# Kernel tuning notes

Measured on AMD Instinct MI355X. Metric: run time of the kernel, lower is better.

Reference implementation:

```python
import jax, jax.numpy as jnp
import numpy as np

ROPE_BASE = 100.0  # CroCo/InfiniteVGGT-style 2D RoPE base

def _rope_1d(sub, pos, base=ROPE_BASE):
    # sub: (B,H,N,half), pos: (B,N) float
    half = sub.shape[-1]
    quarter = half // 2
    inv_freq = 1.0 / (base ** (jnp.arange(quarter, dtype=jnp.float32) / quarter))
    ang = pos[:, None, :, None] * inv_freq  # (B,1,N,quarter)
    cos, sin = jnp.cos(ang), jnp.sin(ang)
    x1, x2 = sub[..., :quarter], sub[..., quarter:]
    return jnp.concatenate([x1 * cos - x2 * sin, x1 * sin + x2 * cos], axis=-1)

def rope_2d(t, positions):
    # t: (B,H,N,Dh); positions: (B,N,2) int (y,x)
    Dh = t.shape[-1]
    half = Dh // 2
    pos_f = positions.astype(t.dtype)
    y = _rope_1d(t[..., :half], pos_f[..., 0])
    x = _rope_1d(t[..., half:], pos_f[..., 1])
    return jnp.concatenate([y, x], axis=-1)

def setup_inputs() -> dict:
    key = jax.random.key(0)
    k1, k2, k3, k4 = jax.random.split(key, 4)
    B, N, C, H = 2, 2048, 1024, 16
    x = jax.random.normal(k1, (B, N, C), dtype=jnp.float32)
    positions = jax.random.randint(k2, (B, N, 2), 0, 64, dtype=jnp.int32)
    qkv_w = jax.random.normal(k3, (3 * C, C), dtype=jnp.float32) * (C ** -0.5)
    proj_w = jax.random.normal(k4, (C, C), dtype=jnp.float32) * (C ** -0.5)
    proj_b = jnp.zeros((C,), dtype=jnp.float32)
    return {"x": x, "positions": positions, "qkv_w": qkv_w, "proj_w": proj_w, "proj_b": proj_b}

def reference(x, positions, qkv_w, proj_w, proj_b):
    B, N, C = x.shape
    H = 16
    Dh = C // H
    scale = Dh ** -0.5
    qkv = (x @ qkv_w.T).reshape(B, N, 3, H, Dh).transpose(2, 0, 3, 1, 4)  # (3,B,H,N,Dh)
    q, k, v = qkv[0], qkv[1], qkv[2]
    q = rope_2d(q, positions)
    k = rope_2d(k, positions)
    attn = jnp.einsum('bhnd,bhmd->bhnm', q, k) * scale  # (B,H,N,N)
    attn = jax.nn.softmax(attn, axis=-1)
    out = jnp.einsum('bhnm,bhmd->bhnd', attn, v)  # (B,H,N,Dh)
    out = out.transpose(0, 2, 1, 3).reshape(B, N, C)
    return out @ proj_w.T + proj_b
```

## Files before the change

### kernel.cpp

```cpp
#include <hip/hip_runtime.h>
#include <cmath>

typedef unsigned short u16;
typedef unsigned int   u32;
typedef __attribute__((ext_vector_type(8))) __bf16 bf16x8;
typedef __attribute__((ext_vector_type(2))) __bf16 bf16x2;
typedef __attribute__((ext_vector_type(4))) float  f32x4;
typedef __attribute__((ext_vector_type(2))) unsigned int u32x2;

constexpr int BB = 2, SEQ = 2048, CH = 1024, NH = 16, DH = 64;

__device__ inline u16 f2bf(float f) {
    u32 u = __builtin_bit_cast(u32, f);
    u += 0x7FFF + ((u >> 16) & 1);
    return (u16)(u >> 16);
}
__device__ inline float bf2f(u16 b) { return __builtin_bit_cast(float, (u32)b << 16); }
__device__ inline u32 pkbf(float a, float b) {
#if __has_builtin(__builtin_amdgcn_cvt_pk_bf16_f32)
    bf16x2 r = __builtin_amdgcn_cvt_pk_bf16_f32(a, b);
    return __builtin_bit_cast(u32, r);
#else
    return (u32)f2bf(a) | ((u32)f2bf(b) << 16);
#endif
}
__device__ inline float fexp2(float x) {
#if __has_builtin(__builtin_amdgcn_exp2f)
    return __builtin_amdgcn_exp2f(x);
#else
    return exp2f(x);
#endif
}

__device__ inline void pl32swap(u32& a, u32& b) {
#if __has_builtin(__builtin_amdgcn_permlane32_swap)
    u32x2 r = __builtin_amdgcn_permlane32_swap(a, b, false, false);
    a = r.x; b = r.y;
#else
    const int ln = threadIdx.x & 63;
    u32 ax = (u32)__shfl_xor((int)a, 32), bx = (u32)__shfl_xor((int)b, 32);
    u32 na = (ln & 32) ? bx : a;
    u32 nb = (ln & 32) ? b : ax;
    a = na; b = nb;
#endif
}
__device__ inline void pl16swap(u32& a, u32& b) {
#if __has_builtin(__builtin_amdgcn_permlane16_swap)
    u32x2 r = __builtin_amdgcn_permlane16_swap(a, b, false, false);
    a = r.x; b = r.y;
#else
    const int ln = threadIdx.x & 63;
    u32 ax = (u32)__shfl_xor((int)a, 16), bx = (u32)__shfl_xor((int)b, 16);
    u32 na = (ln & 16) ? bx : a;
    u32 nb = (ln & 16) ? b : ax;
    a = na; b = nb;
#endif
}

__device__ inline void gld_lds16(const void* g, void* l) {
    __builtin_amdgcn_global_load_lds((const __attribute__((address_space(1))) void*)g,
                                     (__attribute__((address_space(3))) void*)l, 16, 0, 0);
}
__device__ inline f32x4 mfma16(bf16x8 a, bf16x8 b, f32x4 c) {
    return __builtin_amdgcn_mfma_f32_16x16x32_bf16(a, b, c, 0, 0, 0);
}
__device__ inline bf16x8 ld_frag(const u16* p) {
    return __builtin_bit_cast(bf16x8, *(const uint4*)p);
}

__global__ __launch_bounds__(256) void convert_kernel(const float* __restrict__ x,
                                                      const float* __restrict__ wq,
                                                      const float* __restrict__ wp,
                                                      u16* __restrict__ xb,
                                                      u16* __restrict__ wqb,
                                                      u16* __restrict__ wpb,
                                                      float2* __restrict__ tabq,
                                                      float2* __restrict__ tabk) {
    const int q = blockIdx.x * 256 + threadIdx.x;
    if (q >= 2097152) {
        const int idx = q - 2097152;
        if (idx < 1024) {
            const int p = idx >> 4, i = idx & 15;
            const float f = exp2f(-(float)i * 0.41524101186092f);
            float s, c;
            sincosf((float)p * f, &s, &c);
            tabk[idx] = make_float2(c, s);
            tabq[idx] = make_float2(c * 0.18033688011112042f,
                                    s * 0.18033688011112042f);
        }
        return;
    }
    const float* src; u16* dst; int idx;
    if (q < 1048576)            { src = x;  dst = xb;  idx = q; }
    else if (q < 1048576+786432){ src = wq; dst = wqb; idx = q - 1048576; }
    else                        { src = wp; dst = wpb; idx = q - 1048576 - 786432; }
    float4 v = *(const float4*)(src + (size_t)idx * 4);
    ushort4 o; o.x = f2bf(v.x); o.y = f2bf(v.y); o.z = f2bf(v.z); o.w = f2bf(v.w);
    *(ushort4*)(dst + (size_t)idx * 4) = o;
}

__global__ __launch_bounds__(256) void gemm_qkv_rope(const u16* __restrict__ A,
                                                     const u16* __restrict__ Bw,
                                                     const int* __restrict__ pos,
                                                     const float2* __restrict__ tabq,
                                                     const float2* __restrict__ tabk,
                                                     u16* __restrict__ Qb,
                                                     u16* __restrict__ Kb,
                                                     u16* __restrict__ Vt) {
    __shared__ u16 smem[18432];
    const int t = threadIdx.x, lane = t & 63, w = t >> 6;
    const int l15 = lane & 15, quad = lane >> 4;
    const int wm = w >> 1, wn = w & 1;
    const int m0 = blockIdx.y * 128, n0 = blockIdx.x * 128;
    const int K = CH;

    const int row0 = t >> 2, v0 = t & 3;
    const int gi0 = (v0 - (row0 >> 1)) & 3;
    const int row1 = row0 + 64;
    const int gi1 = (v0 - (row1 >> 1)) & 3;

    const u16* A0 = A  + (size_t)(m0 + row0) * K + gi0 * 8;
    const u16* A1 = A  + (size_t)(m0 + row1) * K + gi1 * 8;
    const u16* B0 = Bw + (size_t)(n0 + row0) * K + gi0 * 8;
    const u16* B1 = Bw + (size_t)(n0 + row1) * K + gi1 * 8;

    gld_lds16(A0, smem + t * 8);
    gld_lds16(A1, smem + 2048 + t * 8);
    gld_lds16(B0, smem + 8192 + t * 8);
    gld_lds16(B1, smem + 10240 + t * 8);

    f32x4 acc[4][4] = {};
    for (int kt = 0; kt < K / 32; ++kt) {
        __syncthreads();
        const int cur = (kt & 1) * 4096;
        if (kt + 1 < K / 32) {
            const int off = (kt + 1) * 32;
            const int nxt = ((kt + 1) & 1) * 4096;
            gld_lds16(A0 + off, smem + nxt + t * 8);
            gld_lds16(A1 + off, smem + nxt + 2048 + t * 8);
            gld_lds16(B0 + off, smem + 8192 + nxt + t * 8);
            gld_lds16(B1 + off, smem + 8192 + nxt + 2048 + t * 8);
        }
        const u16* as = smem + cur;
        const u16* bs = smem + 8192 + cur;
        bf16x8 af[4], bfv[4];
#pragma unroll
        for (int mi = 0; mi < 4; ++mi) {
            const int r = wm * 64 + mi * 16 + l15;
            af[mi] = ld_frag(as + (r * 4 + ((quad + (r >> 1)) & 3)) * 8);
        }
#pragma unroll
        for (int nj = 0; nj < 4; ++nj) {
            const int r = wn * 64 + nj * 16 + l15;
            bfv[nj] = ld_frag(bs + (r * 4 + ((quad + (r >> 1)) & 3)) * 8);
        }
#pragma unroll
        for (int mi = 0; mi < 4; ++mi)
#pragma unroll
            for (int nj = 0; nj < 4; ++nj)
                acc[mi][nj] = mfma16(af[mi], bfv[nj], acc[mi][nj]);
    }

    const int reg = n0 >> 10;
    const int h   = ((n0 & 1023) >> 6) + wn;
    __syncthreads();
    u16* T = smem + w * 4608;
    const int rsel = lane >> 3, csel = lane & 7;
    if (reg < 2) {
        const float2* tab = reg ? tabk : tabq;
        u16* dstb = reg ? Kb : Qb;
#pragma unroll
        for (int mi = 0; mi < 4; ++mi) {
#pragma unroll
            for (int r = 0; r < 4; ++r) {
                const int m = m0 + wm * 64 + mi * 16 + quad * 4 + r;
                const int2 pp = *(const int2*)(pos + m * 2);
                const float2 ty = tab[pp.x * 16 + l15];
                const float2 tx = tab[pp.y * 16 + l15];
                const float x1 = acc[mi][0][r], x2 = acc[mi][1][r];
                const float y1 = acc[mi][2][r], y2 = acc[mi][3][r];
                const int ml = (mi * 16 + quad * 4 + r) * 72;
                T[ml + l15]      = f2bf(x1 * ty.x - x2 * ty.y);
                T[ml + l15 + 16] = f2bf(x1 * ty.y + x2 * ty.x);
                T[ml + l15 + 32] = f2bf(y1 * tx.x - y2 * tx.y);
                T[ml + l15 + 48] = f2bf(y1 * tx.y + y2 * tx.x);
            }
        }
        const int mbase = m0 + wm * 64;
        const int bh = (mbase >> 11) * NH + h;
        const int nbase = mbase & 2047;
#pragma unroll
        for (int j = 0; j < 8; ++j) {
            const int row = rsel + j * 8;
            u16* gp = dstb + ((size_t)bh * SEQ + nbase + row) * 64 + csel * 8;
            *(uint4*)gp = *(const uint4*)&T[row * 72 + csel * 8];
        }
    } else {
#pragma unroll
        for (int mi = 0; mi < 4; ++mi)
#pragma unroll
            for (int nj = 0; nj < 4; ++nj)
#pragma unroll
                for (int r = 0; r < 4; ++r)
                    T[(nj * 16 + l15) * 72 + mi * 16 + quad * 4 + r] =
                        f2bf(acc[mi][nj][r]);
        const int bh = (m0 >> 11) * NH + h;
        const int nbase = (m0 & 2047) + wm * 64;
#pragma unroll
        for (int j = 0; j < 8; ++j) {
            const int d = rsel + j * 8;
            u16* gp = Vt + ((size_t)bh * 64 + d) * SEQ + nbase + csel * 8;
            *(uint4*)gp = *(const uint4*)&T[d * 72 + csel * 8];
        }
    }
}

__global__ __launch_bounds__(256, 4) void attn_mfma(const u16* __restrict__ Qb,
                                                    const u16* __restrict__ Kb,
                                                    const u16* __restrict__ Vt,
                                                    u16* __restrict__ Opart,
                                                    float* __restrict__ lpart) {
    __shared__ u16 Ks[2][4096];
    __shared__ u16 Vs[2][4096];
    const int t = threadIdx.x, lane = t & 63, w = t >> 6;
    const int l15 = lane & 15, quad = lane >> 4;
    const int bh = blockIdx.y;
    const int q0 = blockIdx.x * 128;
    const int z  = blockIdx.z;

    const int rowA = t >> 3, vA = t & 7;
    const int giA = (vA - rowA) & 7;
    const int rowB = rowA + 32;
    const int giB = (vA - rowB) & 7;

    const size_t kbase = (size_t)bh * SEQ * 64;
    const size_t vbase = (size_t)bh * 64 * SEQ;

    const uint4 ones_u = {0x3F803F80u, 0x3F803F80u, 0x3F803F80u, 0x3F803F80u};
    const bf16x8 onesf = __builtin_bit_cast(bf16x8, ones_u);

    bf16x8 aq[2][2];
#pragma unroll
    for (int mi = 0; mi < 2; ++mi)
#pragma unroll
        for (int ks = 0; ks < 2; ++ks)
            aq[mi][ks] = ld_frag(Qb + ((size_t)bh * SEQ + q0 + w * 32 + mi * 16 + l15) * 64
                                 + ks * 32 + quad * 8);

#define STAGE(kt_, buf_)                                                          \
    {                                                                             \
        const int k0_ = z * 1024 + (kt_) * 64;                                    \
        gld_lds16(Kb + kbase + (size_t)(k0_ + rowA) * 64 + giA * 8,               \
                  &Ks[buf_][t * 8]);                                              \
        gld_lds16(Kb + kbase + (size_t)(k0_ + rowB) * 64 + giB * 8,               \
                  &Ks[buf_][2048 + t * 8]);                                       \
        gld_lds16(Vt + vbase + (size_t)rowA * SEQ + k0_ + giA * 8,                \
                  &Vs[buf_][t * 8]);                                              \
        gld_lds16(Vt + vbase + (size_t)rowB * SEQ + k0_ + giB * 8,                \
                  &Vs[buf_][2048 + t * 8]);                                       \
    }

    STAGE(0, 0)

    f32x4 oacc[2][4] = {};
    f32x4 lacc[2] = {};

    for (int kt = 0; kt < 16; ++kt) {
        __syncthreads();
        if (kt + 1 < 16) STAGE(kt + 1, (kt + 1) & 1)
        const u16* ksm = Ks[kt & 1];
        const u16* vsm = Vs[kt & 1];

        f32x4 sacc[2][4] = {};
        __builtin_amdgcn_s_setprio(1);
#pragma unroll
        for (int ks = 0; ks < 2; ++ks)
#pragma unroll
            for (int nk = 0; nk < 4; ++nk) {
                const int rK = nk * 16 + l15;
                const bf16x8 kf = ld_frag(ksm + (rK * 8 + (((ks * 4 + quad) + rK) & 7)) * 8);
                sacc[0][nk] = mfma16(kf, aq[0][ks], sacc[0][nk]);
                sacc[1][nk] = mfma16(kf, aq[1][ks], sacc[1][nk]);
            }
        __builtin_amdgcn_s_setprio(0);

        bf16x8 pa[2][2];
#pragma unroll
        for (int mi = 0; mi < 2; ++mi) {
            u32 W[4][2];
#pragma unroll
            for (int nk = 0; nk < 4; ++nk) {
                const float p0 = fexp2(sacc[mi][nk][0]);
                const float p1 = fexp2(sacc[mi][nk][1]);
                const float p2 = fexp2(sacc[mi][nk][2]);
                const float p3 = fexp2(sacc[mi][nk][3]);
                W[nk][0] = pkbf(p0, p1);
                W[nk][1] = pkbf(p2, p3);
            }
            u32 t0[4], t1[4];
            {
                u32 a = W[0][0], c = W[1][0];
                pl32swap(a, c); pl16swap(a, c);
                t0[0] = a; t0[2] = c;
            }
            {
                u32 a = W[0][1], c = W[1][1];
                pl32swap(a, c); pl16swap(a, c);
                t0[1] = a; t0[3] = c;
            }
            {
                u32 a = W[2][0], c = W[3][0];
                pl32swap(a, c); pl16swap(a, c);
                t1[0] = a; t1[2] = c;
            }
            {
                u32 a = W[2][1], c = W[3][1];
                pl32swap(a, c); pl16swap(a, c);
                t1[1] = a; t1[3] = c;
            }
            uint4 u0; u0.x = t0[0]; u0.y = t0[1]; u0.z = t0[2]; u0.w = t0[3];
            uint4 u1; u1.x = t1[0]; u1.y = t1[1]; u1.z = t1[2]; u1.w = t1[3];
            pa[mi][0] = __builtin_bit_cast(bf16x8, u0);
            pa[mi][1] = __builtin_bit_cast(bf16x8, u1);
        }

        __builtin_amdgcn_s_setprio(1);
        lacc[0] = mfma16(pa[0][0], onesf, lacc[0]);
        lacc[0] = mfma16(pa[0][1], onesf, lacc[0]);
        lacc[1] = mfma16(pa[1][0], onesf, lacc[1]);
        lacc[1] = mfma16(pa[1][1], onesf, lacc[1]);
#pragma unroll
        for (int ks = 0; ks < 2; ++ks)
#pragma unroll
            for (int nj = 0; nj < 4; ++nj) {
                const int rV = nj * 16 + l15;
                const bf16x8 vf = ld_frag(vsm + (rV * 8 + (((ks * 4 + quad) + rV) & 7)) * 8);
                oacc[0][nj] = mfma16(pa[0][ks], vf, oacc[0][nj]);
                oacc[1][nj] = mfma16(pa[1][ks], vf, oacc[1][nj]);
            }
        __builtin_amdgcn_s_setprio(0);
    }
#undef STAGE

#pragma unroll
    for (int mi = 0; mi < 2; ++mi)
#pragma unroll
        for (int r = 0; r < 4; ++r) {
            const int qrow = q0 + w * 32 + mi * 16 + quad * 4 + r;
            if (l15 == 0)
                lpart[((size_t)z * 32 + bh) * SEQ + qrow] = lacc[mi][r];
            const size_t orow = (((size_t)z * 32 + bh) * SEQ + qrow) * 64;
#pragma unroll
            for (int nj = 0; nj < 4; ++nj)
                Opart[orow + nj * 16 + l15] = f2bf(oacc[mi][nj][r]);
        }
}

__global__ __launch_bounds__(256) void merge_kernel(const u16* __restrict__ Opart,
                                                    const float* __restrict__ lpart,
                                                    u16* __restrict__ Ob) {
    const int gid = blockIdx.x * 256 + threadIdx.x;
    const int d4 = gid & 15, q = (gid >> 4) & 2047, bh = gid >> 15;
    const size_t i1 = ((size_t)bh * SEQ + q) * 64 + d4 * 4;
    const size_t i2 = i1 + (size_t)32 * SEQ * 64;
    const float inv = 1.0f / (lpart[(size_t)bh * SEQ + q] +
                              lpart[(size_t)(32 + bh) * SEQ + q]);
    const ushort4 a = *(const ushort4*)(Opart + i1);
    const ushort4 b = *(const ushort4*)(Opart + i2);
    ushort4 o;
    o.x = f2bf((bf2f(a.x) + bf2f(b.x)) * inv);
    o.y = f2bf((bf2f(a.y) + bf2f(b.y)) * inv);
    o.z = f2bf((bf2f(a.z) + bf2f(b.z)) * inv);
    o.w = f2bf((bf2f(a.w) + bf2f(b.w)) * inv);
    const int b_ = bh >> 4, h = bh & 15;
    *(ushort4*)(Ob + ((size_t)(b_ * SEQ + q)) * CH + h * 64 + d4 * 4) = o;
}

__global__ __launch_bounds__(256) void gemm_proj(const u16* __restrict__ A,
                                                 const u16* __restrict__ Bw,
                                                 const float* __restrict__ bias,
                                                 float* __restrict__ C) {
    __shared__ u16 smem[12288];
    const int t = threadIdx.x, lane = t & 63, w = t >> 6;
    const int l15 = lane & 15, quad = lane >> 4;
    const int wm = w >> 1, wn = w & 1;
    const int m0 = blockIdx.y * 64, n0 = blockIdx.x * 128;
    const int K = CH, N = CH;

    const int row0 = t >> 2, v0 = t & 3;
    const int gi0 = (v0 - (row0 >> 1)) & 3;
    const int row1 = row0 + 64;
    const int gi1 = (v0 - (row1 >> 1)) & 3;

    const u16* A0 = A  + (size_t)(m0 + row0) * K + gi0 * 8;
    const u16* B0 = Bw + (size_t)(n0 + row0) * K + gi0 * 8;
    const u16* B1 = Bw + (size_t)(n0 + row1) * K + gi1 * 8;

    gld_lds16(A0, smem + t * 8);
    gld_lds16(B0, smem + 4096 + t * 8);
    gld_lds16(B1, smem + 4096 + 2048 + t * 8);

    f32x4 acc[2][4] = {};
    for (int kt = 0; kt < K / 32; ++kt) {
        __syncthreads();
        const int curA = (kt & 1) * 2048;
        const int curB = 4096 + (kt & 1) * 4096;
        if (kt + 1 < K / 32) {
            const int off = (kt + 1) * 32;
            const int nxtA = ((kt + 1) & 1) * 2048;
            const int nxtB = 4096 + ((kt + 1) & 1) * 4096;
            gld_lds16(A0 + off, smem + nxtA + t * 8);
            gld_lds16(B0 + off, smem + nxtB + t * 8);
            gld_lds16(B1 + off, smem + nxtB + 2048 + t * 8);
        }
        const u16* as = smem + curA;
        const u16* bs = smem + curB;
        bf16x8 af[2], bfv[4];
#pragma unroll
        for (int mi = 0; mi < 2; ++mi) {
            const int r = wm * 32 + mi * 16 + l15;
            af[mi] = ld_frag(as + (r * 4 + ((quad + (r >> 1)) & 3)) * 8);
        }
#pragma unroll
        for (int nj = 0; nj < 4; ++nj) {
            const int r = wn * 64 + nj * 16 + l15;
            bfv[nj] = ld_frag(bs + (r * 4 + ((quad + (r >> 1)) & 3)) * 8);
        }
#pragma unroll
        for (int mi = 0; mi < 2; ++mi)
#pragma unroll
            for (int nj = 0; nj < 4; ++nj)
                acc[mi][nj] = mfma16(af[mi], bfv[nj], acc[mi][nj]);
    }
#pragma unroll
    for (int mi = 0; mi < 2; ++mi)
#pragma unroll
        for (int nj = 0; nj < 4; ++nj) {
            const int n = n0 + wn * 64 + nj * 16 + l15;
            const float bv = bias[n];
#pragma unroll
            for (int r = 0; r < 4; ++r) {
                const int m = m0 + wm * 32 + mi * 16 + quad * 4 + r;
                C[(size_t)m * N + n] = acc[mi][nj][r] + bv;
            }
        }
}

extern "C" void kernel_launch(void* const* d_in, const int* in_sizes, int n_in,
                              void* d_out, int out_size, void* d_ws, size_t ws_size,
                              hipStream_t stream) {
    const float* x      = (const float*)d_in[0];
    const int*   pos    = (const int*)d_in[1];
    const float* qkv_w  = (const float*)d_in[2];
    const float* proj_w = (const float*)d_in[3];
    const float* proj_b = (const float*)d_in[4];
    float* out = (float*)d_out;

    u16* ws = (u16*)d_ws;
    u16* x_bf    = ws;
    u16* attn_bf = ws;
    u16* wq_bf   = ws + 4194304;
    float* lpart = (float*)(ws + 4194304);
    u16* wp_bf   = ws + 7340032;
    u16* Qb      = ws + 8388608;
    u16* Kb      = ws + 12582912;
    u16* Vt      = ws + 16777216;
    u16* Opart   = ws + 20971520;
    float2* tabq = (float2*)(ws + 20971520);
    float2* tabk = (float2*)(ws + 20971520 + 4096);

    const int M = BB * SEQ;

    convert_kernel<<<8196, 256, 0, stream>>>(x, qkv_w, proj_w, x_bf, wq_bf, wp_bf,
                                             tabq, tabk);
    gemm_qkv_rope<<<dim3(3 * CH / 128, M / 128), 256, 0, stream>>>(
        x_bf, wq_bf, pos, tabq, tabk, Qb, Kb, Vt);
    attn_mfma<<<dim3(SEQ / 128, BB * NH, 2), 256, 0, stream>>>(Qb, Kb, Vt, Opart, lpart);
    merge_kernel<<<4096, 256, 0, stream>>>(Opart, lpart, attn_bf);
    gemm_proj<<<dim3(CH / 128, M / 64), 256, 0, stream>>>(
        attn_bf, wp_bf, proj_b, out);
}
```

Measured before the change: 196.6 us.

## Split attention KV range four ways with XCD-aware block remap and 4-way merge

Splits the attention key/value sequence into four 512-length chunks instead of two, launching 2048 blocks with a flattened index remapped so consecutive blocks spread across groups (likely to match XCD placement and L2 reuse). Partial outputs go to two buffers, one reusing the output tensor as scratch, and the merge kernel now sums four partials and four row sums. It also raises the occupancy hint to 5 blocks per CU. This trades more partial-output traffic and merge work for more parallelism and shorter per-block loops.

```diff
diff --git a/kernel.cpp b/kernel.cpp
--- a/kernel.cpp
+++ b/kernel.cpp
@@ -215,18 +215,24 @@
     }
 }
 
-__global__ __launch_bounds__(256, 4) void attn_mfma(const u16* __restrict__ Qb,
+__global__ __launch_bounds__(256, 5) void attn_mfma(const u16* __restrict__ Qb,
                                                     const u16* __restrict__ Kb,
                                                     const u16* __restrict__ Vt,
-                                                    u16* __restrict__ Opart,
+                                                    u16* __restrict__ Op01,
+                                                    u16* __restrict__ Op23,
                                                     float* __restrict__ lpart) {
     __shared__ u16 Ks[2][4096];
     __shared__ u16 Vs[2][4096];
     const int t = threadIdx.x, lane = t & 63, w = t >> 6;
     const int l15 = lane & 15, quad = lane >> 4;
-    const int bh = blockIdx.y;
-    const int q0 = blockIdx.x * 128;
-    const int z  = blockIdx.z;
+
+    const int id = blockIdx.x;
+    const int c  = id & 7, r = id >> 3;
+    const int j  = r >> 4, xq = r & 15;
+    const int g  = c + 8 * j;
+    const int bh = g & 31;
+    const int z  = g >> 5;
+    const int q0 = xq * 128;
 
     const int rowA = t >> 3, vA = t & 7;
     const int giA = (vA - rowA) & 7;
@@ -249,7 +255,7 @@
 
 #define STAGE(kt_, buf_)                                                          \
     {                                                                             \
-        const int k0_ = z * 1024 + (kt_) * 64;                                    \
+        const int k0_ = z * 512 + (kt_) * 64;                                     \
         gld_lds16(Kb + kbase + (size_t)(k0_ + rowA) * 64 + giA * 8,               \
                   &Ks[buf_][t * 8]);                                              \
         gld_lds16(Kb + kbase + (size_t)(k0_ + rowB) * 64 + giB * 8,               \
@@ -265,9 +271,9 @@
     f32x4 oacc[2][4] = {};
     f32x4 lacc[2] = {};
 
-    for (int kt = 0; kt < 16; ++kt) {
+    for (int kt = 0; kt < 8; ++kt) {
         __syncthreads();
-        if (kt + 1 < 16) STAGE(kt + 1, (kt + 1) & 1)
+        if (kt + 1 < 8) STAGE(kt + 1, (kt + 1) & 1)
         const u16* ksm = Ks[kt & 1];
         const u16* vsm = Vs[kt & 1];
 
@@ -299,24 +305,24 @@
             }
             u32 t0[4], t1[4];
             {
-                u32 a = W[0][0], c = W[1][0];
-                pl32swap(a, c); pl16swap(a, c);
-                t0[0] = a; t0[2] = c;
+                u32 a = W[0][0], cc = W[1][0];
+                pl32swap(a, cc); pl16swap(a, cc);
+                t0[0] = a; t0[2] = cc;
             }
             {
-                u32 a = W[0][1], c = W[1][1];
-                pl32swap(a, c); pl16swap(a, c);
-                t0[1] = a; t0[3] = c;
+                u32 a = W[0][1], cc = W[1][1];
+                pl32swap(a, cc); pl16swap(a, cc);
+                t0[1] = a; t0[3] = cc;
             }
             {
-                u32 a = W[2][0], c = W[3][0];
-                pl32swap(a, c); pl16swap(a, c);
-                t1[0] = a; t1[2] = c;
+                u32 a = W[2][0], cc = W[3][0];
+                pl32swap(a, cc); pl16swap(a, cc);
+                t1[0] = a; t1[2] = cc;
             }
             {
-                u32 a = W[2][1], c = W[3][1];
-                pl32swap(a, c); pl16swap(a, c);
-                t1[1] = a; t1[3] = c;
+                u32 a = W[2][1], cc = W[3][1];
+                pl32swap(a, cc); pl16swap(a, cc);
+                t1[1] = a; t1[3] = cc;
             }
             uint4 u0; u0.x = t0[0]; u0.y = t0[1]; u0.z = t0[2]; u0.w = t0[3];
             uint4 u1; u1.x = t1[0]; u1.y = t1[1]; u1.z = t1[2]; u1.w = t1[3];
@@ -342,6 +348,7 @@
     }
 #undef STAGE
 
+    u16* ob = (z < 2 ? Op01 : Op23) + (size_t)(z & 1) * 4194304;
 #pragma unroll
     for (int mi = 0; mi < 2; ++mi)
 #pragma unroll
@@ -349,29 +356,33 @@
             const int qrow = q0 + w * 32 + mi * 16 + quad * 4 + r;
             if (l15 == 0)
                 lpart[((size_t)z * 32 + bh) * SEQ + qrow] = lacc[mi][r];
-            const size_t orow = (((size_t)z * 32 + bh) * SEQ + qrow) * 64;
+            const size_t orow = ((size_t)bh * SEQ + qrow) * 64;
 #pragma unroll
             for (int nj = 0; nj < 4; ++nj)
-                Opart[orow + nj * 16 + l15] = f2bf(oacc[mi][nj][r]);
-        }
-}
-
-__global__ __launch_bounds__(256) void merge_kernel(const u16* __restrict__ Opart,
+                ob[orow + nj * 16 + l15] = f2bf(oacc[mi][nj][r]);
+        }
+}
+
+__global__ __launch_bounds__(256) void merge_kernel(const u16* __restrict__ Op01,
+                                                    const u16* __restrict__ Op23,
                                                     const float* __restrict__ lpart,
                                                     u16* __restrict__ Ob) {
     const int gid = blockIdx.x * 256 + threadIdx.x;
     const int d4 = gid & 15, q = (gid >> 4) & 2047, bh = gid >> 15;
-    const size_t i1 = ((size_t)bh * SEQ + q) * 64 + d4 * 4;
-    const size_t i2 = i1 + (size_t)32 * SEQ * 64;
+    const size_t ibase = ((size_t)bh * SEQ + q) * 64 + d4 * 4;
     const float inv = 1.0f / (lpart[(size_t)bh * SEQ + q] +
-                              lpart[(size_t)(32 + bh) * SEQ + q]);
-    const ushort4 a = *(const ushort4*)(Opart + i1);
-    const ushort4 b = *(const ushort4*)(Opart + i2);
+                              lpart[((size_t)32 + bh) * SEQ + q] +
+                              lpart[((size_t)64 + bh) * SEQ + q] +
+                              lpart[((size_t)96 + bh) * SEQ + q]);
+    const ushort4 a = *(const ushort4*)(Op01 + ibase);
+    const ushort4 b = *(const ushort4*)(Op01 + ibase + 4194304);
+    const ushort4 cc = *(const ushort4*)(Op23 + ibase);
+    const ushort4 d = *(const ushort4*)(Op23 + ibase + 4194304);
     ushort4 o;
-    o.x = f2bf((bf2f(a.x) + bf2f(b.x)) * inv);
-    o.y = f2bf((bf2f(a.y) + bf2f(b.y)) * inv);
-    o.z = f2bf((bf2f(a.z) + bf2f(b.z)) * inv);
-    o.w = f2bf((bf2f(a.w) + bf2f(b.w)) * inv);
+    o.x = f2bf((bf2f(a.x) + bf2f(b.x) + bf2f(cc.x) + bf2f(d.x)) * inv);
+    o.y = f2bf((bf2f(a.y) + bf2f(b.y) + bf2f(cc.y) + bf2f(d.y)) * inv);
+    o.z = f2bf((bf2f(a.z) + bf2f(b.z) + bf2f(cc.z) + bf2f(d.z)) * inv);
+    o.w = f2bf((bf2f(a.w) + bf2f(b.w) + bf2f(cc.w) + bf2f(d.w)) * inv);
     const int b_ = bh >> 4, h = bh & 15;
     *(ushort4*)(Ob + ((size_t)(b_ * SEQ + q)) * CH + h * 64 + d4 * 4) = o;
 }
@@ -458,14 +469,15 @@
 
     u16* ws = (u16*)d_ws;
     u16* x_bf    = ws;
-    u16* attn_bf = ws;
     u16* wq_bf   = ws + 4194304;
     float* lpart = (float*)(ws + 4194304);
     u16* wp_bf   = ws + 7340032;
     u16* Qb      = ws + 8388608;
+    u16* attn_bf = ws + 8388608;
     u16* Kb      = ws + 12582912;
     u16* Vt      = ws + 16777216;
-    u16* Opart   = ws + 20971520;
+    u16* Op01    = ws + 20971520;
+    u16* Op23    = (u16*)d_out;
     float2* tabq = (float2*)(ws + 20971520);
     float2* tabk = (float2*)(ws + 20971520 + 4096);
 
@@ -475,8 +487,8 @@
                                              tabq, tabk);
     gemm_qkv_rope<<<dim3(3 * CH / 128, M / 128), 256, 0, stream>>>(
         x_bf, wq_bf, pos, tabq, tabk, Qb, Kb, Vt);
-    attn_mfma<<<dim3(SEQ / 128, BB * NH, 2), 256, 0, stream>>>(Qb, Kb, Vt, Opart, lpart);
-    merge_kernel<<<4096, 256, 0, stream>>>(Opart, lpart, attn_bf);
+    attn_mfma<<<2048, 256, 0, stream>>>(Qb, Kb, Vt, Op01, Op23, lpart);
+    merge_kernel<<<4096, 256, 0, stream>>>(Op01, Op23, lpart, attn_bf);
     gemm_proj<<<dim3(CH / 128, M / 64), 256, 0, stream>>>(
         attn_bf, wp_bf, proj_b, out);
 }
```

After: 265.1 us. +34.9%, slower.

## Shrink attention query tile, drop double buffering, remap 1D grid for XCD locality

Applied to the files above, without the earlier changes.

The attention kernel now processes 64 query rows per block instead of 128, with each wave handling 16 rows. It loads K/V tiles into a single LDS buffer with two barriers per iteration instead of double-buffering. The grid becomes a 1D launch of 2048 blocks, with a swizzled index so blocks sharing the same head and split land on the same XCD, and occupancy is raised to 8 blocks per CU. The intent is more waves in flight and better L2 reuse of K/V, at the cost of twice the K/V traffic per query and an exposed load latency with no prefetch.

```diff
diff --git a/kernel.cpp b/kernel.cpp
--- a/kernel.cpp
+++ b/kernel.cpp
@@ -215,18 +215,23 @@
     }
 }
 
-__global__ __launch_bounds__(256, 4) void attn_mfma(const u16* __restrict__ Qb,
+__global__ __launch_bounds__(256, 8) void attn_mfma(const u16* __restrict__ Qb,
                                                     const u16* __restrict__ Kb,
                                                     const u16* __restrict__ Vt,
                                                     u16* __restrict__ Opart,
                                                     float* __restrict__ lpart) {
-    __shared__ u16 Ks[2][4096];
-    __shared__ u16 Vs[2][4096];
+    __shared__ u16 Ks[4096];
+    __shared__ u16 Vs[4096];
     const int t = threadIdx.x, lane = t & 63, w = t >> 6;
     const int l15 = lane & 15, quad = lane >> 4;
-    const int bh = blockIdx.y;
-    const int q0 = blockIdx.x * 128;
-    const int z  = blockIdx.z;
+
+    const int id = blockIdx.x;
+    const int c  = id & 7, r_ = id >> 3;
+    const int j  = r_ >> 5, xq = r_ & 31;
+    const int g  = c + 8 * j;
+    const int bh = g & 31;
+    const int z  = g >> 5;
+    const int q0 = xq * 64;
 
     const int rowA = t >> 3, vA = t & 7;
     const int giA = (vA - rowA) & 7;
@@ -239,121 +244,110 @@
     const uint4 ones_u = {0x3F803F80u, 0x3F803F80u, 0x3F803F80u, 0x3F803F80u};
     const bf16x8 onesf = __builtin_bit_cast(bf16x8, ones_u);
 
-    bf16x8 aq[2][2];
-#pragma unroll
-    for (int mi = 0; mi < 2; ++mi)
-#pragma unroll
-        for (int ks = 0; ks < 2; ++ks)
-            aq[mi][ks] = ld_frag(Qb + ((size_t)bh * SEQ + q0 + w * 32 + mi * 16 + l15) * 64
-                                 + ks * 32 + quad * 8);
-
-#define STAGE(kt_, buf_)                                                          \
+    bf16x8 aq[2];
+#pragma unroll
+    for (int ks = 0; ks < 2; ++ks)
+        aq[ks] = ld_frag(Qb + ((size_t)bh * SEQ + q0 + w * 16 + l15) * 64
+                         + ks * 32 + quad * 8);
+
+#define STAGE(kt_)                                                                \
     {                                                                             \
         const int k0_ = z * 1024 + (kt_) * 64;                                    \
         gld_lds16(Kb + kbase + (size_t)(k0_ + rowA) * 64 + giA * 8,               \
-                  &Ks[buf_][t * 8]);                                              \
+                  &Ks[t * 8]);                                                    \
         gld_lds16(Kb + kbase + (size_t)(k0_ + rowB) * 64 + giB * 8,               \
-                  &Ks[buf_][2048 + t * 8]);                                       \
+                  &Ks[2048 + t * 8]);                                             \
         gld_lds16(Vt + vbase + (size_t)rowA * SEQ + k0_ + giA * 8,                \
-                  &Vs[buf_][t * 8]);                                              \
+                  &Vs[t * 8]);                                                    \
         gld_lds16(Vt + vbase + (size_t)rowB * SEQ + k0_ + giB * 8,                \
-                  &Vs[buf_][2048 + t * 8]);                                       \
-    }
-
-    STAGE(0, 0)
-
-    f32x4 oacc[2][4] = {};
-    f32x4 lacc[2] = {};
+                  &Vs[2048 + t * 8]);                                             \
+    }
+
+    f32x4 oacc[4] = {};
+    f32x4 lacc = {};
 
     for (int kt = 0; kt < 16; ++kt) {
         __syncthreads();
-        if (kt + 1 < 16) STAGE(kt + 1, (kt + 1) & 1)
-        const u16* ksm = Ks[kt & 1];
-        const u16* vsm = Vs[kt & 1];
-
-        f32x4 sacc[2][4] = {};
+        STAGE(kt)
+        __syncthreads();
+
+        f32x4 sacc[4] = {};
         __builtin_amdgcn_s_setprio(1);
 #pragma unroll
         for (int ks = 0; ks < 2; ++ks)
 #pragma unroll
             for (int nk = 0; nk < 4; ++nk) {
                 const int rK = nk * 16 + l15;
-                const bf16x8 kf = ld_frag(ksm + (rK * 8 + (((ks * 4 + quad) + rK) & 7)) * 8);
-                sacc[0][nk] = mfma16(kf, aq[0][ks], sacc[0][nk]);
-                sacc[1][nk] = mfma16(kf, aq[1][ks], sacc[1][nk]);
+                const bf16x8 kf = ld_frag(Ks + (rK * 8 + (((ks * 4 + quad) + rK) & 7)) * 8);
+                sacc[nk] = mfma16(kf, aq[ks], sacc[nk]);
             }
         __builtin_amdgcn_s_setprio(0);
 
-        bf16x8 pa[2][2];
-#pragma unroll
-        for (int mi = 0; mi < 2; ++mi) {
+        bf16x8 pa[2];
+        {
             u32 W[4][2];
 #pragma unroll
             for (int nk = 0; nk < 4; ++nk) {
-                const float p0 = fexp2(sacc[mi][nk][0]);
-                const float p1 = fexp2(sacc[mi][nk][1]);
-                const float p2 = fexp2(sacc[mi][nk][2]);
-                const float p3 = fexp2(sacc[mi][nk][3]);
+                const float p0 = fexp2(sacc[nk][0]);
+                const float p1 = fexp2(sacc[nk][1]);
+                const float p2 = fexp2(sacc[nk][2]);
+                const float p3 = fexp2(sacc[nk][3]);
                 W[nk][0] = pkbf(p0, p1);
                 W[nk][1] = pkbf(p2, p3);
             }
             u32 t0[4], t1[4];
             {
-                u32 a = W[0][0], c = W[1][0];
-                pl32swap(a, c); pl16swap(a, c);
-                t0[0] = a; t0[2] = c;
+                u32 a = W[0][0], cc = W[1][0];
+                pl32swap(a, cc); pl16swap(a, cc);
+                t0[0] = a; t0[2] = cc;
             }
             {
-                u32 a = W[0][1], c = W[1][1];
-                pl32swap(a, c); pl16swap(a, c);
-                t0[1] = a; t0[3] = c;
+                u32 a = W[0][1], cc = W[1][1];
+                pl32swap(a, cc); pl16swap(a, cc);
+                t0[1] = a; t0[3] = cc;
             }
             {
-                u32 a = W[2][0], c = W[3][0];
-                pl32swap(a, c); pl16swap(a, c);
-                t1[0] = a; t1[2] = c;
+                u32 a = W[2][0], cc = W[3][0];
+                pl32swap(a, cc); pl16swap(a, cc);
+                t1[0] = a; t1[2] = cc;
             }
             {
-                u32 a = W[2][1], c = W[3][1];
-                pl32swap(a, c); pl16swap(a, c);
-                t1[1] = a; t1[3] = c;
+                u32 a = W[2][1], cc = W[3][1];
+                pl32swap(a, cc); pl16swap(a, cc);
+                t1[1] = a; t1[3] = cc;
             }
             uint4 u0; u0.x = t0[0]; u0.y = t0[1]; u0.z = t0[2]; u0.w = t0[3];
             uint4 u1; u1.x = t1[0]; u1.y = t1[1]; u1.z = t1[2]; u1.w = t1[3];
-            pa[mi][0] = __builtin_bit_cast(bf16x8, u0);
-            pa[mi][1] = __builtin_bit_cast(bf16x8, u1);
+            pa[0] = __builtin_bit_cast(bf16x8, u0);
+            pa[1] = __builtin_bit_cast(bf16x8, u1);
         }
 
         __builtin_amdgcn_s_setprio(1);
-        lacc[0] = mfma16(pa[0][0], onesf, lacc[0]);
-        lacc[0] = mfma16(pa[0][1], onesf, lacc[0]);
-        lacc[1] = mfma16(pa[1][0], onesf, lacc[1]);
-        lacc[1] = mfma16(pa[1][1], onesf, lacc[1]);
+        lacc = mfma16(pa[0], onesf, lacc);
+        lacc = mfma16(pa[1], onesf, lacc);
 #pragma unroll
         for (int ks = 0; ks < 2; ++ks)
 #pragma unroll
             for (int nj = 0; nj < 4; ++nj) {
                 const int rV = nj * 16 + l15;
-                const bf16x8 vf = ld_frag(vsm + (rV * 8 + (((ks * 4 + quad) + rV) & 7)) * 8);
-                oacc[0][nj] = mfma16(pa[0][ks], vf, oacc[0][nj]);
-                oacc[1][nj] = mfma16(pa[1][ks], vf, oacc[1][nj]);
+                const bf16x8 vf = ld_frag(Vs + (rV * 8 + (((ks * 4 + quad) + rV) & 7)) * 8);
+                oacc[nj] = mfma16(pa[ks], vf, oacc[nj]);
             }
         __builtin_amdgcn_s_setprio(0);
     }
 #undef STAGE
 
-#pragma unroll
-    for (int mi = 0; mi < 2; ++mi)
-#pragma unroll
-        for (int r = 0; r < 4; ++r) {
-            const int qrow = q0 + w * 32 + mi * 16 + quad * 4 + r;
-            if (l15 == 0)
-                lpart[((size_t)z * 32 + bh) * SEQ + qrow] = lacc[mi][r];
-            const size_t orow = (((size_t)z * 32 + bh) * SEQ + qrow) * 64;
-#pragma unroll
-            for (int nj = 0; nj < 4; ++nj)
-                Opart[orow + nj * 16 + l15] = f2bf(oacc[mi][nj][r]);
-        }
+    u16* ob = Opart + (size_t)z * 4194304;
+#pragma unroll
+    for (int r = 0; r < 4; ++r) {
+        const int qrow = q0 + w * 16 + quad * 4 + r;
+        if (l15 == 0)
+            lpart[((size_t)z * 32 + bh) * SEQ + qrow] = lacc[r];
+        const size_t orow = ((size_t)bh * SEQ + qrow) * 64;
+#pragma unroll
+        for (int nj = 0; nj < 4; ++nj)
+            ob[orow + nj * 16 + l15] = f2bf(oacc[nj][r]);
+    }
 }
 
 __global__ __launch_bounds__(256) void merge_kernel(const u16* __restrict__ Opart,
@@ -362,9 +356,9 @@
     const int gid = blockIdx.x * 256 + threadIdx.x;
     const int d4 = gid & 15, q = (gid >> 4) & 2047, bh = gid >> 15;
     const size_t i1 = ((size_t)bh * SEQ + q) * 64 + d4 * 4;
-    const size_t i2 = i1 + (size_t)32 * SEQ * 64;
+    const size_t i2 = i1 + 4194304;
     const float inv = 1.0f / (lpart[(size_t)bh * SEQ + q] +
-                              lpart[(size_t)(32 + bh) * SEQ + q]);
+                              lpart[((size_t)32 + bh) * SEQ + q]);
     const ushort4 a = *(const ushort4*)(Opart + i1);
     const ushort4 b = *(const ushort4*)(Opart + i2);
     ushort4 o;
@@ -475,7 +469,7 @@
                                              tabq, tabk);
     gemm_qkv_rope<<<dim3(3 * CH / 128, M / 128), 256, 0, stream>>>(
         x_bf, wq_bf, pos, tabq, tabk, Qb, Kb, Vt);
-    attn_mfma<<<dim3(SEQ / 128, BB * NH, 2), 256, 0, stream>>>(Qb, Kb, Vt, Opart, lpart);
+    attn_mfma<<<2048, 256, 0, stream>>>(Qb, Kb, Vt, Opart, lpart);
     merge_kernel<<<4096, 256, 0, stream>>>(Opart, lpart, attn_bf);
     gemm_proj<<<dim3(CH / 128, M / 64), 256, 0, stream>>>(
         attn_bf, wp_bf, proj_b, out);
```

Result: slower. 201.5 us (+2.5%).

## Triple-buffer K/V staging in attention and remap blocks for XCD locality

Applied to the files above, without the earlier changes.

The attention kernel moves from double to triple-buffered K/V shared-memory staging. It uses explicit vmcnt waits and a single barrier per iteration, so loads for the next tile overlap compute with less synchronization. It also flattens the grid to 1D and remaps block ids so that blocks sharing the same (bh, split) land together across the 8 XCDs, which should improve L2 reuse of K/V. The extra LDS lowers the launch bound from 4 to 3 blocks per CU, trading occupancy for deeper prefetch.

```diff
diff --git a/kernel.cpp b/kernel.cpp
--- a/kernel.cpp
+++ b/kernel.cpp
@@ -215,18 +215,23 @@
     }
 }
 
-__global__ __launch_bounds__(256, 4) void attn_mfma(const u16* __restrict__ Qb,
+__global__ __launch_bounds__(256, 3) void attn_mfma(const u16* __restrict__ Qb,
                                                     const u16* __restrict__ Kb,
                                                     const u16* __restrict__ Vt,
                                                     u16* __restrict__ Opart,
                                                     float* __restrict__ lpart) {
-    __shared__ u16 Ks[2][4096];
-    __shared__ u16 Vs[2][4096];
+    __shared__ u16 Ks[3][4096];
+    __shared__ u16 Vs[3][4096];
     const int t = threadIdx.x, lane = t & 63, w = t >> 6;
     const int l15 = lane & 15, quad = lane >> 4;
-    const int bh = blockIdx.y;
-    const int q0 = blockIdx.x * 128;
-    const int z  = blockIdx.z;
+
+    const int id = blockIdx.x;
+    const int c  = id & 7, r_ = id >> 3;
+    const int j  = r_ >> 4, xq = r_ & 15;
+    const int g  = c + 8 * j;
+    const int bh = g & 31;
+    const int z  = g >> 5;
+    const int q0 = xq * 128;
 
     const int rowA = t >> 3, vA = t & 7;
     const int giA = (vA - rowA) & 7;
@@ -265,11 +270,20 @@
     f32x4 oacc[2][4] = {};
     f32x4 lacc[2] = {};
 
+    int rb = 0;
     for (int kt = 0; kt < 16; ++kt) {
-        __syncthreads();
-        if (kt + 1 < 16) STAGE(kt + 1, (kt + 1) & 1)
-        const u16* ksm = Ks[kt & 1];
-        const u16* vsm = Vs[kt & 1];
+        const int sb = (rb + 1 == 3) ? 0 : rb + 1;
+        if (kt + 1 < 16) {
+            STAGE(kt + 1, sb)
+            asm volatile("s_waitcnt vmcnt(4)" ::: "memory");
+        } else {
+            asm volatile("s_waitcnt vmcnt(0)" ::: "memory");
+        }
+        __builtin_amdgcn_sched_barrier(0);
+        __builtin_amdgcn_s_barrier();
+        __builtin_amdgcn_sched_barrier(0);
+        const u16* ksm = Ks[rb];
+        const u16* vsm = Vs[rb];
 
         f32x4 sacc[2][4] = {};
         __builtin_amdgcn_s_setprio(1);
@@ -299,24 +313,24 @@
             }
             u32 t0[4], t1[4];
             {
-                u32 a = W[0][0], c = W[1][0];
-                pl32swap(a, c); pl16swap(a, c);
-                t0[0] = a; t0[2] = c;
+                u32 a = W[0][0], cc = W[1][0];
+                pl32swap(a, cc); pl16swap(a, cc);
+                t0[0] = a; t0[2] = cc;
             }
             {
-                u32 a = W[0][1], c = W[1][1];
-                pl32swap(a, c); pl16swap(a, c);
-                t0[1] = a; t0[3] = c;
+                u32 a = W[0][1], cc = W[1][1];
+                pl32swap(a, cc); pl16swap(a, cc);
+                t0[1] = a; t0[3] = cc;
             }
             {
-                u32 a = W[2][0], c = W[3][0];
-                pl32swap(a, c); pl16swap(a, c);
-                t1[0] = a; t1[2] = c;
+                u32 a = W[2][0], cc = W[3][0];
+                pl32swap(a, cc); pl16swap(a, cc);
+                t1[0] = a; t1[2] = cc;
             }
             {
-                u32 a = W[2][1], c = W[3][1];
-                pl32swap(a, c); pl16swap(a, c);
-                t1[1] = a; t1[3] = c;
+                u32 a = W[2][1], cc = W[3][1];
+                pl32swap(a, cc); pl16swap(a, cc);
+                t1[1] = a; t1[3] = cc;
             }
             uint4 u0; u0.x = t0[0]; u0.y = t0[1]; u0.z = t0[2]; u0.w = t0[3];
             uint4 u1; u1.x = t1[0]; u1.y = t1[1]; u1.z = t1[2]; u1.w = t1[3];
@@ -339,9 +353,11 @@
                 oacc[1][nj] = mfma16(pa[1][ks], vf, oacc[1][nj]);
             }
         __builtin_amdgcn_s_setprio(0);
+        rb = sb;
     }
 #undef STAGE
 
+    u16* ob = Opart + (size_t)z * 4194304;
 #pragma unroll
     for (int mi = 0; mi < 2; ++mi)
 #pragma unroll
@@ -349,10 +365,10 @@
             const int qrow = q0 + w * 32 + mi * 16 + quad * 4 + r;
             if (l15 == 0)
                 lpart[((size_t)z * 32 + bh) * SEQ + qrow] = lacc[mi][r];
-            const size_t orow = (((size_t)z * 32 + bh) * SEQ + qrow) * 64;
+            const size_t orow = ((size_t)bh * SEQ + qrow) * 64;
 #pragma unroll
             for (int nj = 0; nj < 4; ++nj)
-                Opart[orow + nj * 16 + l15] = f2bf(oacc[mi][nj][r]);
+                ob[orow + nj * 16 + l15] = f2bf(oacc[mi][nj][r]);
         }
 }
 
@@ -362,9 +378,9 @@
     const int gid = blockIdx.x * 256 + threadIdx.x;
     const int d4 = gid & 15, q = (gid >> 4) & 2047, bh = gid >> 15;
     const size_t i1 = ((size_t)bh * SEQ + q) * 64 + d4 * 4;
-    const size_t i2 = i1 + (size_t)32 * SEQ * 64;
+    const size_t i2 = i1 + 4194304;
     const float inv = 1.0f / (lpart[(size_t)bh * SEQ + q] +
-                              lpart[(size_t)(32 + bh) * SEQ + q]);
+                              lpart[((size_t)32 + bh) * SEQ + q]);
     const ushort4 a = *(const ushort4*)(Opart + i1);
     const ushort4 b = *(const ushort4*)(Opart + i2);
     ushort4 o;
@@ -475,7 +491,7 @@
                                              tabq, tabk);
     gemm_qkv_rope<<<dim3(3 * CH / 128, M / 128), 256, 0, stream>>>(
         x_bf, wq_bf, pos, tabq, tabk, Qb, Kb, Vt);
-    attn_mfma<<<dim3(SEQ / 128, BB * NH, 2), 256, 0, stream>>>(Qb, Kb, Vt, Opart, lpart);
+    attn_mfma<<<1024, 256, 0, stream>>>(Qb, Kb, Vt, Opart, lpart);
     merge_kernel<<<4096, 256, 0, stream>>>(Opart, lpart, attn_bf);
     gemm_proj<<<dim3(CH / 128, M / 64), 256, 0, stream>>>(
         attn_bf, wp_bf, proj_b, out);
```

New measurement: 199.4 us. About the same (+1.4%).
